# Kernel tuning notes

Hardware: AMD Instinct MI355X
Metric: run time of the kernel (lower is better)

The kernel has to match this reference:

```python
import jax, jax.numpy as jnp
import numpy as np

B, N, LATENT, HIDDEN = 65536, 32, 32, 64

def setup_inputs() -> dict:
    key = jax.random.key(0)
    ks = jax.random.split(key, 16)
    def xavier(k, shape):
        fan_in, fan_out = shape[1], shape[0]
        lim = float(np.sqrt(6.0 / (fan_in + fan_out)))
        return jax.random.uniform(k, shape, jnp.float32, -lim, lim)
    inp = {
        'x_sensors': jax.random.normal(ks[0], (B, N), jnp.float32),
        'state_x': jax.random.uniform(ks[1], (B, 1), jnp.float32),
        # GAT: W Linear(1, LATENT, bias=False), a Linear(2*LATENT, 1, bias=False), xavier init
        'W_gat': xavier(ks[2], (LATENT, 1)),
        'a_gat': xavier(ks[3], (1, 2 * LATENT)),
        # pooling: Linear(LATENT, LATENT//2) -> Tanh -> Linear(LATENT//2, 1) -> Softmax(dim=1)
        'p1_w': xavier(ks[4], (LATENT // 2, LATENT)),
        'p1_b': jnp.zeros((LATENT // 2,), jnp.float32),
        'p2_w': xavier(ks[5], (1, LATENT // 2)),
        'p2_b': jnp.zeros((1,), jnp.float32),
        # MNN: MonotonicLinear raw weights uniform(-0.5, 0.5), zero bias
        'm1_w': jax.random.uniform(ks[6], (HIDDEN, 1), jnp.float32, -0.5, 0.5),
        'm1_b': jnp.zeros((HIDDEN,), jnp.float32),
        'm2_w': jax.random.uniform(ks[7], (HIDDEN, HIDDEN), jnp.float32, -0.5, 0.5),
        'm2_b': jnp.zeros((HIDDEN,), jnp.float32),
        'm3_w': jax.random.uniform(ks[8], (LATENT, HIDDEN), jnp.float32, -0.5, 0.5),
        'm3_b': jnp.zeros((LATENT,), jnp.float32),
    }
    return inp

def reference(x_sensors, state_x, W_gat, a_gat, p1_w, p1_b, p2_w, p2_b,
              m1_w, m1_b, m2_w, m2_b, m3_w, m3_b):
    # --- GAT encoder ---
    # h = x_sensors[..., None] (B,N,1); Wh = h @ W_gat.T -> (B,N,D)
    Wh = jnp.einsum('bn,d->bnd', x_sensors, W_gat[:, 0])
    # e_ij = leakyrelu(a^T [Wh_i || Wh_j]) decomposed: a = [a1; a2]
    a1, a2 = a_gat[0, :LATENT], a_gat[0, LATENT:]
    s_i = jnp.einsum('bnd,d->bn', Wh, a1)  # contribution of Wh_i
    s_j = jnp.einsum('bnd,d->bn', Wh, a2)  # contribution of Wh_j
    e = jax.nn.leaky_relu(s_i[:, :, None] + s_j[:, None, :], 0.2)  # (B,N,N)
    alpha = jax.nn.softmax(e, axis=2)  # dropout is identity in eval
    h_prime = jnp.einsum('bij,bjd->bid', alpha, Wh)  # (B,N,D)
    # pooling: softmax over sensor dim (dim=1)
    t = jnp.tanh(h_prime @ p1_w.T + p1_b)
    beta = jax.nn.softmax(t @ p2_w.T + p2_b, axis=1)  # (B,N,1)
    z_enc = jnp.sum(h_prime * beta, axis=1)  # (B,D)
    # --- MNN decoder (exp-positive weights) ---
    h1 = jnp.tanh(state_x @ jnp.exp(m1_w).T + m1_b)
    h2 = jnp.tanh(h1 @ jnp.exp(m2_w).T + m2_b)
    z_dec = h2 @ jnp.exp(m3_w).T + m3_b  # (B,D)
    return (z_enc, z_dec)
```

## Files before the change

### kernel.cpp

```cpp
#include <hip/hip_runtime.h>
#include <hip/hip_bf16.h>

#define LOG2E     1.4426950408889634f
#define TWO_LOG2E 2.8853900817779268f

typedef __attribute__((ext_vector_type(8))) _Float16 f16x8;
typedef __attribute__((ext_vector_type(4))) float    f32x4;
typedef __attribute__((ext_vector_type(2))) float    f32x2;

__device__ __forceinline__ float rcp_(float x){ return __builtin_amdgcn_rcpf(x); }
__device__ __forceinline__ float ex2_(float x){ return __builtin_amdgcn_exp2f(x); }

template<int K>
__device__ __forceinline__ float quadbc(float v){
  constexpr int ctrl = K * 0x55;
  return __int_as_float(__builtin_amdgcn_mov_dpp(__float_as_int(v), ctrl, 0xf, 0xf, true));
}

union FragH { f16x8 v; uint32_t w[4]; uint4 u4; };

__device__ __forceinline__ uint32_t pkh(float a, float b){
  union { _Float16 h; uint16_t u; } ca, cb;
  ca.h = (_Float16)a; cb.h = (_Float16)b;
  return (uint32_t)ca.u | ((uint32_t)cb.u << 16);
}
__device__ __forceinline__ void exph8(const float* __restrict__ src, FragH& out){
  float4 a = *(const float4*)src;
  float4 b = *(const float4*)(src + 4);
  out.w[0] = pkh(__expf(a.x), __expf(a.y));
  out.w[1] = pkh(__expf(a.z), __expf(a.w));
  out.w[2] = pkh(__expf(b.x), __expf(b.y));
  out.w[3] = pkh(__expf(b.z), __expf(b.w));
}

#define TBL_N     256
#define TBL_SCALE 12.8f
#define TBL_LO    -10.0f
#define TBL_CMAX  9.9f

#define ATT_J(JQ, JR) { \
    const float Fj_ = quadbc<JQ>(Fjr[JR]); \
    const float Fq_ = quadbc<JQ>(Fqr[JR]); \
    const float xj_ = quadbc<JQ>(xi[JR]); \
    const f32x2 Fj2_ = {Fj_,Fj_}, Fq2_ = {Fq_,Fq_}, xj2_ = {xj_,xj_}; \
    f32x2 pe_; \
    pe_ = __builtin_elementwise_max(Ei2[0]*Fj2_, Eq2[0]*Fq2_); s2[0] = s2[0] + pe_; sx2[0] = sx2[0] + pe_*xj2_; \
    pe_ = __builtin_elementwise_max(Ei2[1]*Fj2_, Eq2[1]*Fq2_); s2[1] = s2[1] + pe_; sx2[1] = sx2[1] + pe_*xj2_; \
    pe_ = __builtin_elementwise_max(Ei2[2]*Fj2_, Eq2[2]*Fq2_); s2[2] = s2[2] + pe_; sx2[2] = sx2[2] + pe_*xj2_; \
    pe_ = __builtin_elementwise_max(Ei2[3]*Fj2_, Eq2[3]*Fq2_); s2[3] = s2[3] + pe_; sx2[3] = sx2[3] + pe_*xj2_; \
  }
#define ATT_Q(JQ) ATT_J(JQ,0) ATT_J(JQ,1) ATT_J(JQ,2) ATT_J(JQ,3) \
                  ATT_J(JQ,4) ATT_J(JQ,5) ATT_J(JQ,6) ATT_J(JQ,7)

__global__ __launch_bounds__(256, 4) void IDSSM_main(
    const float* __restrict__ xs,  const float* __restrict__ stx,
    const float* __restrict__ Wg,  const float* __restrict__ ag,
    const float* __restrict__ p1w, const float* __restrict__ p1b,
    const float* __restrict__ p2w, const float* __restrict__ p2b,
    const float* __restrict__ m1w, const float* __restrict__ m1b,
    const float* __restrict__ m2w, const float* __restrict__ m2b,
    const float* __restrict__ m3w, const float* __restrict__ m3b,
    float* __restrict__ out, int B)
{
  __shared__ uint4 fgl[768];
  __shared__ float tbl[TBL_N];
  __shared__ float qsh[16], pbb[16], p2wn[16], scal[3];

  const int tid = threadIdx.x;
  const int lb  = tid >> 2;
  const int q   = tid & 3;
  const int b0  = blockIdx.x * 64;
  const int b   = b0 + lb;
  const bool valid = (b < B);
  const int rsrc = valid ? b : (B - 1);

  const float4* xrow4 = (const float4*)(xs + (size_t)rsrc*32);
  const float4 xia = xrow4[q*2], xib = xrow4[q*2 + 1];
  float xi[8] = { xia.x, xia.y, xia.z, xia.w, xib.x, xib.y, xib.z, xib.w };

  #pragma unroll
  for (int rep = 0; rep < 3; ++rep){
    const int s    = tid + rep*256;
    const int slot = s >> 6;
    const int l    = s & 63;
    const int bl_  = l & 15;
    const int gt_  = l >> 4;
    const float* src;
    if (slot < 8) src = m2w + (bl_ + 16*(slot>>1))*64 + 8*gt_ + 32*(slot&1);
    else { const int s2 = slot - 8;
           src = m3w + (bl_ + 16*(s2>>1))*64 + 8*gt_ + 32*(s2&1); }
    FragH h;
    exph8(src, h);
    fgl[slot*64 + l] = h.u4;
  }
  if (tid >= 64 && tid < 80){
    const int k = tid - 64;
    float acc = 0.f;
    #pragma unroll
    for (int d = 0; d < 32; ++d) acc += p1w[k*32 + d] * Wg[d];
    qsh[k]  = acc * TWO_LOG2E;
    pbb[k]  = p1b[k] * TWO_LOG2E;
    p2wn[k] = -2.f * p2w[k];
  }
  if (tid == 80){
    float A1 = 0.f, A2 = 0.f;
    #pragma unroll
    for (int d = 0; d < 32; ++d){ A1 += Wg[d]*ag[d]; A2 += Wg[d]*ag[32+d]; }
    scal[0] = A1 * LOG2E;
    scal[1] = A2 * LOG2E;
  }
  if (tid == 81){
    float sp = 0.f;
    #pragma unroll
    for (int k = 0; k < 16; ++k) sp += p2w[k];
    scal[2] = sp + p2b[0];
  }
  __syncthreads();

  {
    const float c = TBL_LO + (float)tid * (1.0f/TBL_SCALE);
    float u = scal[2];
    #pragma unroll
    for (int k = 0; k < 16; ++k){
      float E = ex2_(fmaf(c, qsh[k], pbb[k]));
      u = fmaf(p2wn[k], rcp_(E + 1.f), u);
    }
    tbl[tid] = u * LOG2E;
  }

  const float A1p = scal[0], A2p = scal[1];
  float Fjr[8], Fqr[8];
  #pragma unroll
  for (int t = 0; t < 8; ++t){
    const float tv = A2p * xi[t];
    Fjr[t] = ex2_(tv);
    Fqr[t] = ex2_(0.2f * tv);
  }
  f32x2 Ei2[4], Eq2[4], s2[4], sx2[4];
  #pragma unroll
  for (int p = 0; p < 4; ++p){
    const float sa = A1p * xi[2*p], sb = A1p * xi[2*p + 1];
    Ei2[p] = (f32x2){ ex2_(sa), ex2_(sb) };
    Eq2[p] = (f32x2){ ex2_(0.2f*sa), ex2_(0.2f*sb) };
    s2[p]  = (f32x2)(0.f);
    sx2[p] = (f32x2)(0.f);
  }
  ATT_Q(0) ATT_Q(1) ATT_Q(2) ATT_Q(3)

  __syncthreads();

  float Zs = 0.f, Zd = 0.f;
  #pragma unroll
  for (int p = 0; p < 4; ++p){
    #pragma unroll
    for (int h = 0; h < 2; ++h){
      const float sv  = h ? s2[p].y  : s2[p].x;
      const float sxv = h ? sx2[p].y : sx2[p].x;
      const float c  = sxv * rcp_(sv);
      const float cc = fminf(fmaxf(c, TBL_LO), TBL_CMAX);
      const float f  = (cc - TBL_LO) * TBL_SCALE;
      const int   n  = (int)f;
      const float fr = f - (float)n;
      const float t0 = tbl[n];
      const float t1 = tbl[n + 1];
      const float eb = ex2_(fmaf(fr, t1 - t0, t0));
      Zs = fmaf(eb, c, Zs);
      Zd += eb;
    }
  }
  Zs += __shfl_xor(Zs, 1);  Zd += __shfl_xor(Zd, 1);
  Zs += __shfl_xor(Zs, 2);  Zd += __shfl_xor(Zd, 2);
  const float Z = Zs * rcp_(Zd);

  if (valid){
    const float4 w0 = ((const float4*)Wg)[q*2 + 0];
    const float4 w1 = ((const float4*)Wg)[q*2 + 1];
    float4* o = (float4*)(out + (size_t)b*32 + q*8);
    o[0] = make_float4(Z*w0.x, Z*w0.y, Z*w0.z, Z*w0.w);
    o[1] = make_float4(Z*w1.x, Z*w1.y, Z*w1.z, Z*w1.w);
  }

  const int lane = tid & 63;
  const int wv   = tid >> 6;
  const int gt   = lane >> 4;
  const int bl   = lane & 15;
  const int bd   = b0 + wv*16 + bl;
  const float sx0 = stx[(bd < B) ? bd : (B-1)];

  FragH h1f[2];
  #pragma unroll
  for (int kt = 0; kt < 2; ++kt){
    const int g0 = 8*gt + 32*kt;
    const float4* w1p = (const float4*)(m1w + g0);
    const float4* b1p = (const float4*)(m1b + g0);
    float4 wa = w1p[0], wb = w1p[1];
    float4 ba = b1p[0], bb = b1p[1];
    float wv8[8] = { wa.x,wa.y,wa.z,wa.w, wb.x,wb.y,wb.z,wb.w };
    float bv8[8] = { ba.x,ba.y,ba.z,ba.w, bb.x,bb.y,bb.z,bb.w };
    float hv[8];
    #pragma unroll
    for (int j = 0; j < 8; ++j){
      const float e1 = ex2_(wv8[j] * LOG2E) * TWO_LOG2E;
      const float E  = ex2_(fmaf(sx0, e1, bv8[j] * TWO_LOG2E));
      hv[j] = fmaf(-2.f, rcp_(E + 1.f), 1.f);
    }
    #pragma unroll
    for (int jw = 0; jw < 4; ++jw)
      h1f[kt].w[jw] = pkh(hv[2*jw], hv[2*jw+1]);
  }

  f32x4 acc[4];
  #pragma unroll
  for (int mt = 0; mt < 4; ++mt){
    float4 bi = *(const float4*)(m2b + 16*mt + 4*gt);
    acc[mt][0]=bi.x; acc[mt][1]=bi.y; acc[mt][2]=bi.z; acc[mt][3]=bi.w;
  }
  #pragma unroll
  for (int mt = 0; mt < 4; ++mt){
    #pragma unroll
    for (int kt = 0; kt < 2; ++kt){
      FragH A; A.u4 = fgl[(mt*2 + kt)*64 + lane];
      acc[mt] = __builtin_amdgcn_mfma_f32_16x16x32_f16(A.v, h1f[kt].v, acc[mt], 0, 0, 0);
    }
  }

  uint32_t Wp[4][2];
  #pragma unroll
  for (int mt = 0; mt < 4; ++mt){
    float t0 = fmaf(-2.f, rcp_(ex2_(acc[mt][0]*TWO_LOG2E) + 1.f), 1.f);
    float t1 = fmaf(-2.f, rcp_(ex2_(acc[mt][1]*TWO_LOG2E) + 1.f), 1.f);
    float t2 = fmaf(-2.f, rcp_(ex2_(acc[mt][2]*TWO_LOG2E) + 1.f), 1.f);
    float t3 = fmaf(-2.f, rcp_(ex2_(acc[mt][3]*TWO_LOG2E) + 1.f), 1.f);
    Wp[mt][0] = pkh(t0, t1);
    Wp[mt][1] = pkh(t2, t3);
  }

  FragH B2[2];
  const int hiSel = gt >> 1;
  #pragma unroll
  for (int kt2 = 0; kt2 < 2; ++kt2){
    #pragma unroll
    for (int jw = 0; jw < 4; ++jw){
      const int sl = bl + 16*(((jw>>1) + 2*gt) & 3);
      const int w  = jw & 1;
      uint32_t c0 = (uint32_t)__shfl((int)Wp[2*kt2+0][w], sl);
      uint32_t c1 = (uint32_t)__shfl((int)Wp[2*kt2+1][w], sl);
      B2[kt2].w[jw] = hiSel ? c1 : c0;
    }
  }

  f32x4 acc2[2];
  #pragma unroll
  for (int mt2 = 0; mt2 < 2; ++mt2){
    float4 bi = *(const float4*)(m3b + 16*mt2 + 4*gt);
    acc2[mt2][0]=bi.x; acc2[mt2][1]=bi.y; acc2[mt2][2]=bi.z; acc2[mt2][3]=bi.w;
  }
  #pragma unroll
  for (int mt2 = 0; mt2 < 2; ++mt2){
    #pragma unroll
    for (int kt2 = 0; kt2 < 2; ++kt2){
      FragH A; A.u4 = fgl[512 + (mt2*2 + kt2)*64 + lane];
      acc2[mt2] = __builtin_amdgcn_mfma_f32_16x16x32_f16(A.v, B2[kt2].v, acc2[mt2], 0, 0, 0);
    }
  }

  if (bd < B){
    float* o = out + (size_t)B*32 + (size_t)bd*32;
    *(float4*)(o + 4*gt)      = make_float4(acc2[0][0], acc2[0][1], acc2[0][2], acc2[0][3]);
    *(float4*)(o + 16 + 4*gt) = make_float4(acc2[1][0], acc2[1][1], acc2[1][2], acc2[1][3]);
  }
}

extern "C" void kernel_launch(void* const* d_in, const int* in_sizes, int n_in,
                              void* d_out, int out_size, void* d_ws, size_t ws_size,
                              hipStream_t stream)
{
  const float* xs  = (const float*)d_in[0];
  const float* stx = (const float*)d_in[1];
  const float* Wg  = (const float*)d_in[2];
  const float* ag  = (const float*)d_in[3];
  const float* p1w = (const float*)d_in[4];
  const float* p1b = (const float*)d_in[5];
  const float* p2w = (const float*)d_in[6];
  const float* p2b = (const float*)d_in[7];
  const float* m1w = (const float*)d_in[8];
  const float* m1b = (const float*)d_in[9];
  const float* m2w = (const float*)d_in[10];
  const float* m2b = (const float*)d_in[11];
  const float* m3w = (const float*)d_in[12];
  const float* m3b = (const float*)d_in[13];
  float* out = (float*)d_out;
  const int B = in_sizes[0] / 32;
  const int nblk = (B + 63) / 64;
  hipLaunchKernelGGL(IDSSM_main, dim3(nblk), dim3(256), 0, stream,
                     xs, stx, Wg, ag, p1w, p1b, p2w, p2b,
                     m1w, m1b, m2w, m2b, m3w, m3b, out, B);
}
```

Baseline: 24.21 us.

## Split each batch row across eight lanes and halve rows per block

Result: slower. 57.42 us (+137.1%).

```diff
diff --git a/kernel.cpp b/kernel.cpp
--- a/kernel.cpp
+++ b/kernel.cpp
@@ -38,7 +38,7 @@
 #define TBL_LO    -10.0f
 #define TBL_CMAX  9.9f
 
-#define ATT_J(JQ, JR) { \
+#define EATT_J(JQ, JR) { \
     const float Fj_ = quadbc<JQ>(Fjr[JR]); \
     const float Fq_ = quadbc<JQ>(Fqr[JR]); \
     const float xj_ = quadbc<JQ>(xi[JR]); \
@@ -46,13 +46,11 @@
     f32x2 pe_; \
     pe_ = __builtin_elementwise_max(Ei2[0]*Fj2_, Eq2[0]*Fq2_); s2[0] = s2[0] + pe_; sx2[0] = sx2[0] + pe_*xj2_; \
     pe_ = __builtin_elementwise_max(Ei2[1]*Fj2_, Eq2[1]*Fq2_); s2[1] = s2[1] + pe_; sx2[1] = sx2[1] + pe_*xj2_; \
-    pe_ = __builtin_elementwise_max(Ei2[2]*Fj2_, Eq2[2]*Fq2_); s2[2] = s2[2] + pe_; sx2[2] = sx2[2] + pe_*xj2_; \
-    pe_ = __builtin_elementwise_max(Ei2[3]*Fj2_, Eq2[3]*Fq2_); s2[3] = s2[3] + pe_; sx2[3] = sx2[3] + pe_*xj2_; \
-  }
-#define ATT_Q(JQ) ATT_J(JQ,0) ATT_J(JQ,1) ATT_J(JQ,2) ATT_J(JQ,3) \
-                  ATT_J(JQ,4) ATT_J(JQ,5) ATT_J(JQ,6) ATT_J(JQ,7)
-
-__global__ __launch_bounds__(256, 4) void IDSSM_main(
+  }
+#define EATT_Q(JQ) EATT_J(JQ,0) EATT_J(JQ,1) EATT_J(JQ,2) EATT_J(JQ,3)
+#define EATT_ALL   EATT_Q(0) EATT_Q(1) EATT_Q(2) EATT_Q(3)
+
+__global__ __launch_bounds__(256, 8) void IDSSM_main(
     const float* __restrict__ xs,  const float* __restrict__ stx,
     const float* __restrict__ Wg,  const float* __restrict__ ag,
     const float* __restrict__ p1w, const float* __restrict__ p1b,
@@ -67,16 +65,15 @@
   __shared__ float qsh[16], pbb[16], p2wn[16], scal[3];
 
   const int tid = threadIdx.x;
-  const int lb  = tid >> 2;
-  const int q   = tid & 3;
-  const int b0  = blockIdx.x * 64;
+  const int lb  = tid >> 3;
+  const int r   = tid & 7;
+  const int b0  = blockIdx.x * 32;
   const int b   = b0 + lb;
   const bool valid = (b < B);
   const int rsrc = valid ? b : (B - 1);
 
-  const float4* xrow4 = (const float4*)(xs + (size_t)rsrc*32);
-  const float4 xia = xrow4[q*2], xib = xrow4[q*2 + 1];
-  float xi[8] = { xia.x, xia.y, xia.z, xia.w, xib.x, xib.y, xib.z, xib.w };
+  const float4 xv = *(const float4*)(xs + (size_t)rsrc*32 + r*4);
+  float xi[4] = { xv.x, xv.y, xv.z, xv.w };
 
   #pragma unroll
   for (int rep = 0; rep < 3; ++rep){
@@ -129,29 +126,36 @@
   }
 
   const float A1p = scal[0], A2p = scal[1];
-  float Fjr[8], Fqr[8];
-  #pragma unroll
-  for (int t = 0; t < 8; ++t){
+  float Fjr[4], Fqr[4];
+  #pragma unroll
+  for (int t = 0; t < 4; ++t){
     const float tv = A2p * xi[t];
     Fjr[t] = ex2_(tv);
     Fqr[t] = ex2_(0.2f * tv);
   }
-  f32x2 Ei2[4], Eq2[4], s2[4], sx2[4];
-  #pragma unroll
-  for (int p = 0; p < 4; ++p){
+  f32x2 Ei2[2], Eq2[2], s2[2], sx2[2];
+  #pragma unroll
+  for (int p = 0; p < 2; ++p){
     const float sa = A1p * xi[2*p], sb = A1p * xi[2*p + 1];
     Ei2[p] = (f32x2){ ex2_(sa), ex2_(sb) };
     Eq2[p] = (f32x2){ ex2_(0.2f*sa), ex2_(0.2f*sb) };
     s2[p]  = (f32x2)(0.f);
     sx2[p] = (f32x2)(0.f);
   }
-  ATT_Q(0) ATT_Q(1) ATT_Q(2) ATT_Q(3)
+  EATT_ALL
+  #pragma unroll
+  for (int t = 0; t < 4; ++t){
+    xi[t]  = __shfl_xor(xi[t], 4);
+    Fjr[t] = __shfl_xor(Fjr[t], 4);
+    Fqr[t] = __shfl_xor(Fqr[t], 4);
+  }
+  EATT_ALL
 
   __syncthreads();
 
   float Zs = 0.f, Zd = 0.f;
   #pragma unroll
-  for (int p = 0; p < 4; ++p){
+  for (int p = 0; p < 2; ++p){
     #pragma unroll
     for (int h = 0; h < 2; ++h){
       const float sv  = h ? s2[p].y  : s2[p].x;
@@ -170,18 +174,19 @@
   }
   Zs += __shfl_xor(Zs, 1);  Zd += __shfl_xor(Zd, 1);
   Zs += __shfl_xor(Zs, 2);  Zd += __shfl_xor(Zd, 2);
+  Zs += __shfl_xor(Zs, 4);  Zd += __shfl_xor(Zd, 4);
   const float Z = Zs * rcp_(Zd);
 
   if (valid){
-    const float4 w0 = ((const float4*)Wg)[q*2 + 0];
-    const float4 w1 = ((const float4*)Wg)[q*2 + 1];
-    float4* o = (float4*)(out + (size_t)b*32 + q*8);
-    o[0] = make_float4(Z*w0.x, Z*w0.y, Z*w0.z, Z*w0.w);
-    o[1] = make_float4(Z*w1.x, Z*w1.y, Z*w1.z, Z*w1.w);
-  }
+    const float4 w = ((const float4*)Wg)[r];
+    *(float4*)(out + (size_t)b*32 + r*4) =
+        make_float4(Z*w.x, Z*w.y, Z*w.z, Z*w.w);
+  }
+
+  const int wv = tid >> 6;
+  if (wv >= 2) return;
 
   const int lane = tid & 63;
-  const int wv   = tid >> 6;
   const int gt   = lane >> 4;
   const int bl   = lane & 15;
   const int bd   = b0 + wv*16 + bl;
@@ -291,7 +296,7 @@
   const float* m3b = (const float*)d_in[13];
   float* out = (float*)d_out;
   const int B = in_sizes[0] / 32;
-  const int nblk = (B + 63) / 64;
+  const int nblk = (B + 31) / 32;
   hipLaunchKernelGGL(IDSSM_main, dim3(nblk), dim3(256), 0, stream,
                      xs, stx, Wg, ag, p1w, p1b, p2w, p2b,
                      m1w, m1b, m2w, m2b, m3w, m3b, out, B);
```
